# Kernel tuning notes

Hardware: AMD Instinct MI355X
Metric: run time of the kernel (lower is better)

## Reference

```python
import jax, jax.numpy as jnp
import numpy as np

NUM_HEADS = 8  # from init_kwargs


def setup_inputs() -> dict:
    key = jax.random.key(0)
    ks = jax.random.split(key, 8)
    B, N, Din, H, Dout, E = 4, 2048, 256, 512, 256, 65536
    s = 0.02
    return {
        "x": jax.random.normal(ks[0], (B, N, Din), jnp.float32),
        "edge_index": jax.random.randint(ks[1], (2, E), 0, N),
        "W_gcn": jax.random.normal(ks[2], (Din, H), jnp.float32) * s,
        "b_gcn": jnp.zeros((H,), jnp.float32),
        "in_proj_w": jax.random.normal(ks[3], (3 * H, H), jnp.float32) * s,
        "in_proj_b": jnp.zeros((3 * H,), jnp.float32),
        "out_proj_w": jax.random.normal(ks[4], (H, H), jnp.float32) * s,
        "out_proj_b": jnp.zeros((H,), jnp.float32),
        "fc_w": jax.random.normal(ks[5], (H, Dout), jnp.float32) * s,
        "fc_b": jnp.zeros((Dout,), jnp.float32),
    }


def _gcn(x, edge_index, W, b):
    # PyG GCNConv: add self-loops, symmetric normalization, gather-scatter aggregation.
    B, N, _ = x.shape
    loop = jnp.arange(N)
    src = jnp.concatenate([edge_index[0], loop])  # message source j
    dst = jnp.concatenate([edge_index[1], loop])  # aggregation target i
    deg = jnp.zeros((N,), x.dtype).at[dst].add(1.0)
    dinv = jnp.where(deg > 0, jax.lax.rsqrt(deg), 0.0)
    norm = dinv[src] * dinv[dst]                  # [Etot]
    xl = x @ W                                    # [B, N, H]
    msgs = xl[:, src, :] * norm[None, :, None]    # [B, Etot, H]
    out = jnp.zeros_like(xl).at[:, dst].add(msgs)  # scatter-add over edges
    return out + b


def _mha(x_nbh, wi, bi, wo, bo, nh):
    # torch MultiheadAttention, input [N(seq), B, H], self-attention.
    N, B, H = x_nbh.shape
    dh = H // nh
    qkv = x_nbh @ wi.T + bi                       # [N, B, 3H]
    q, k, v = jnp.split(qkv, 3, axis=-1)
    q = q.reshape(N, B, nh, dh) * (dh ** -0.5)
    k = k.reshape(N, B, nh, dh)
    v = v.reshape(N, B, nh, dh)
    scores = jnp.einsum("nbhd,mbhd->bhnm", q, k)  # [B, nh, N, N]
    attn = jax.nn.softmax(scores, axis=-1)
    o = jnp.einsum("bhnm,mbhd->nbhd", attn, v).reshape(N, B, H)
    return o @ wo.T + bo


def reference(x, edge_index, W_gcn, b_gcn, in_proj_w, in_proj_b,
              out_proj_w, out_proj_b, fc_w, fc_b):
    h = _gcn(x, edge_index, W_gcn, b_gcn)         # [B, N, H]
    h = jnp.transpose(h, (1, 0, 2))               # [N, B, H]
    h = _mha(h, in_proj_w, in_proj_b, out_proj_w, out_proj_b, NUM_HEADS)
    h = jnp.transpose(h, (1, 0, 2))               # [B, N, H]
    h = jax.nn.relu(h)
    return h @ fc_w + fc_b                        # [B, N, Dout]
```

## Files before the change

### kernel.cpp

```cpp
#include <hip/hip_runtime.h>
#include <hip/hip_bf16.h>


#define NN 2048
#define HH 512
#define NHEAD 8
#define DH 64

typedef _Float16 f16;
typedef __attribute__((ext_vector_type(2))) _Float16 f16x2;
typedef __attribute__((ext_vector_type(4))) _Float16 f16x4;
typedef __attribute__((ext_vector_type(8))) _Float16 f16x8;
typedef __attribute__((ext_vector_type(4))) float f32x4;

#define GLOAD_LDS16(g, l)                                              \
  __builtin_amdgcn_global_load_lds(                                    \
      (const __attribute__((address_space(1))) void*)(g),              \
      (__attribute__((address_space(3))) void*)(l), 16, 0, 0)


__global__ __launch_bounds__(256) void prep_cvt_kernel(const float* __restrict__ wi,
                                                       const float* __restrict__ wo,
                                                       f16* __restrict__ wi16,
                                                       f16* __restrict__ wo16,
                                                       float* __restrict__ deg,
                                                       int* __restrict__ cursor) {
  const int bid = blockIdx.x, t = threadIdx.x;
  if (bid < 768) {
    const int i = bid * 256 + t;
    const float4 v = ((const float4*)wi)[i];
    f16x4 o = { (f16)v.x, (f16)v.y, (f16)v.z, (f16)v.w };
    ((f16x4*)wi16)[i] = o;
  } else if (bid < 1024) {
    const int i = (bid - 768) * 256 + t;
    const float4 v = ((const float4*)wo)[i];
    f16x4 o = { (f16)v.x, (f16)v.y, (f16)v.z, (f16)v.w };
    ((f16x4*)wo16)[i] = o;
  } else {
    for (int i = t; i < NN; i += 256) { deg[i] = 1.0f; cursor[i] = 0; }
  }
}

__global__ __launch_bounds__(256) void prep_transpose_kernel(const float* __restrict__ wg,
                                                             const float* __restrict__ fcw,
                                                             f16* __restrict__ wg16t,
                                                             f16* __restrict__ fcw16t) {
  __shared__ float tbuf[32][33];
  const float* in;
  f16* outp;
  int R, C, bx, by;
  if (blockIdx.x < 128) { in = wg;  outp = wg16t;  R = 256; C = 512;
                          bx = blockIdx.x & 15; by = blockIdx.x >> 4; }
  else { int id = blockIdx.x - 128; in = fcw; outp = fcw16t; R = 512; C = 256;
         bx = id & 7; by = id >> 3; }
  const int c0 = bx * 32, r0 = by * 32;
  const int tx = threadIdx.x & 31, ty = threadIdx.x >> 5;
#pragma unroll
  for (int i = 0; i < 32; i += 8) tbuf[ty + i][tx] = in[(size_t)(r0 + ty + i) * C + c0 + tx];
  __syncthreads();
#pragma unroll
  for (int i = 0; i < 32; i += 8)
    outp[(size_t)(c0 + ty + i) * R + r0 + tx] = (f16)tbuf[tx][ty + i];
}


__global__ __launch_bounds__(256) void count_deg_kernel(const int* __restrict__ ei, int E,
                                                        float* __restrict__ deg) {
  int e = blockIdx.x * 256 + threadIdx.x;
  if (e < E) atomicAdd(&deg[ei[E + e]], 1.0f);
}

__global__ __launch_bounds__(1024) void build_rowptr_kernel(const float* __restrict__ deg,
                                                            float* __restrict__ dinv,
                                                            int* __restrict__ rowptr) {
  __shared__ int a[NN];
  __shared__ int bbuf[NN];
  const int t = threadIdx.x;
  for (int i = t; i < NN; i += 1024) {
    float dg = deg[i];
    a[i] = (int)dg - 1;
    dinv[i] = rsqrtf(dg);
  }
  __syncthreads();
  int* src = a;
  int* dst = bbuf;
  for (int off = 1; off < NN; off <<= 1) {
    for (int i = t; i < NN; i += 1024) {
      int v = src[i];
      if (i >= off) v += src[i - off];
      dst[i] = v;
    }
    __syncthreads();
    int* tmp = src; src = dst; dst = tmp;
  }
  for (int i = t; i < NN; i += 1024) rowptr[i + 1] = src[i];
  if (t == 0) rowptr[0] = 0;
}

__global__ __launch_bounds__(256) void fill_csr_kernel(const int* __restrict__ ei, int E,
                                                       const int* __restrict__ rowptr,
                                                       int* __restrict__ cursor,
                                                       int* __restrict__ csr_src) {
  int e = blockIdx.x * 256 + threadIdx.x;
  if (e < E) {
    int s = ei[e];
    int d = ei[E + e];
    int pos = atomicAdd(&cursor[d], 1);
    csr_src[rowptr[d] + pos] = s;
  }
}


template <int OUTMODE, bool BIAS, bool RELU, bool AF32, int MT = 128>
__global__ __launch_bounds__(256) void mfma_gemm_kernel(
    const void* __restrict__ Ap, const f16* __restrict__ Bt,
    const float* __restrict__ bias, void* __restrict__ Cout,
    int M, int N, int K,
    f16* __restrict__ q_out, f16* __restrict__ k_out, f16* __restrict__ v_out) {
  constexpr int MI = MT / 32;
  __shared__ f16 As[MT * 32];
  __shared__ f16 Bs[128 * 32];
  const int tid = threadIdx.x;
  const int wave = tid >> 6, lane = tid & 63;
  const int quad = lane >> 4, l16 = lane & 15;
  const int m0 = blockIdx.y * MT, n0 = blockIdx.x * 128;
  const int moff = (wave >> 1) * (MI * 16), noff = (wave & 1) * 64;

  f32x4 acc[MI][4];
#pragma unroll
  for (int i = 0; i < MI; ++i)
#pragma unroll
    for (int j = 0; j < 4; ++j) acc[i][j] = (f32x4){0.f, 0.f, 0.f, 0.f};

  const int rpw = MT / 4;
  const int srowA = rpw * wave + (lane >> 2);
  const int srowB = 32 * wave + (lane >> 2);
  const int kch = (lane & 3) * 8;
  const f16* Ag = (const f16*)Ap + (size_t)(m0 + srowA) * K + kch;
  const float* Ag32 = (const float*)Ap + (size_t)(m0 + srowA) * K + kch;
  const f16* Bg = Bt + (size_t)(n0 + srowB) * K + kch;
  f16* As_w = &As[(rpw * wave) * 32];
  f16* Bs_w = &Bs[(32 * wave) * 32];

  for (int k0 = 0; k0 < K; k0 += 32) {
    __syncthreads();
    if (AF32) {
#pragma unroll
      for (int t = 0; t < 2; ++t) {
        const float* g = Ag32 + k0 + (size_t)(16 * t) * K;
        const float4 u0 = *(const float4*)g;
        const float4 u1 = *(const float4*)(g + 4);
        f16x8 o = { (f16)u0.x, (f16)u0.y, (f16)u0.z, (f16)u0.w,
                    (f16)u1.x, (f16)u1.y, (f16)u1.z, (f16)u1.w };
        *(f16x8*)&As[(srowA + 16 * t) * 32 + kch] = o;
      }
    } else {
      GLOAD_LDS16(Ag + k0, As_w);
      if (MT == 128) GLOAD_LDS16(Ag + k0 + (size_t)16 * K, As_w + 16 * 32);
    }
    GLOAD_LDS16(Bg + k0, Bs_w);
    GLOAD_LDS16(Bg + k0 + (size_t)16 * K, Bs_w + 16 * 32);
    __syncthreads();
    f16x8 af[MI], bf[4];
#pragma unroll
    for (int m16 = 0; m16 < MI; ++m16)
      af[m16] = *(const f16x8*)&As[(moff + m16 * 16 + l16) * 32 + quad * 8];
#pragma unroll
    for (int n16 = 0; n16 < 4; ++n16)
      bf[n16] = *(const f16x8*)&Bs[(noff + n16 * 16 + l16) * 32 + quad * 8];
#pragma unroll
    for (int m16 = 0; m16 < MI; ++m16)
#pragma unroll
      for (int n16 = 0; n16 < 4; ++n16)
        acc[m16][n16] =
            __builtin_amdgcn_mfma_f32_16x16x32_f16(af[m16], bf[n16], acc[m16][n16], 0, 0, 0);
  }

  float bv[4];
#pragma unroll
  for (int n16 = 0; n16 < 4; ++n16)
    bv[n16] = BIAS ? bias[n0 + noff + n16 * 16 + l16] : 0.f;

  if (OUTMODE == 2) {
    const int hblk = (n0 >> 6) + (wave & 1);
    const int which = hblk >> 3, h = hblk & 7;
    f16* dst = (which == 0) ? q_out : (which == 1) ? k_out : v_out;
    const float scale = (which == 0) ? 0.125f : 1.0f;
#pragma unroll
    for (int m16 = 0; m16 < MI; ++m16) {
#pragma unroll
      for (int r = 0; r < 4; ++r) {
        const int m = m0 + moff + m16 * 16 + quad * 4 + r;
        const int b = m >> 11, ns = m & 2047;
        f16* row = dst + ((size_t)(b * 8 + h) * NN + ns) * DH;
#pragma unroll
        for (int n16 = 0; n16 < 4; ++n16) {
          const int d = n16 * 16 + l16;
          row[d] = (f16)((acc[m16][n16][r] + bv[n16]) * scale);
        }
      }
    }
  } else {
#pragma unroll
    for (int m16 = 0; m16 < MI; ++m16) {
#pragma unroll
      for (int r = 0; r < 4; ++r) {
        const size_t row = (size_t)(m0 + moff + m16 * 16 + quad * 4 + r) * N;
#pragma unroll
        for (int n16 = 0; n16 < 4; ++n16) {
          const int col = n0 + noff + n16 * 16 + l16;
          float v = acc[m16][n16][r] + bv[n16];
          if (RELU) v = fmaxf(v, 0.f);
          if (OUTMODE == 0) ((float*)Cout)[row + col] = v;
          else ((f16*)Cout)[row + col] = (f16)v;
        }
      }
    }
  }
}


__global__ __launch_bounds__(256) void gcn_aggregate_kernel(const f16* __restrict__ xl,
                                                            const float* __restrict__ dinv,
                                                            const int* __restrict__ rowptr,
                                                            const int* __restrict__ csr_src,
                                                            const float* __restrict__ b_gcn,
                                                            f16* __restrict__ out) {
  __shared__ int s_src[256];
  __shared__ float s_dv[256];
  const int i = blockIdx.x;
  const int tid = threadIdx.x;
  const float dv_i = dinv[i];
  const int f = tid * 2;
  float ax[4], ay[4];
#pragma unroll
  for (int b = 0; b < 4; ++b) {
    const f16x2 self = *(const f16x2*)&xl[((size_t)(b * NN) + i) * HH + f];
    ax[b] = (float)self.x * dv_i;
    ay[b] = (float)self.y * dv_i;
  }
  const int beg = rowptr[i], end = rowptr[i + 1];
  for (int c0 = beg; c0 < end; c0 += 256) {
    const int cnt = min(256, end - c0);
    __syncthreads();
    if (tid < cnt) {
      int s = csr_src[c0 + tid];
      s_src[tid] = s;
      s_dv[tid] = dinv[s];
    }
    __syncthreads();
    for (int t = 0; t < cnt; ++t) {
      const int row = s_src[t];
      const float w = s_dv[t];
#pragma unroll
      for (int b = 0; b < 4; ++b) {
        const f16x2 v = *(const f16x2*)&xl[((size_t)(b * NN) + row) * HH + f];
        ax[b] = fmaf((float)v.x, w, ax[b]);
        ay[b] = fmaf((float)v.y, w, ay[b]);
      }
    }
  }
  const float2 bg = *(const float2*)&b_gcn[f];
#pragma unroll
  for (int b = 0; b < 4; ++b) {
    f16x2 o = { (f16)(ax[b] * dv_i + bg.x), (f16)(ay[b] * dv_i + bg.y) };
    *(f16x2*)&out[((size_t)(b * NN) + i) * HH + f] = o;
  }
}


__global__ __launch_bounds__(256) void flash_attn_f16_kernel(const f16* __restrict__ Qb,
                                                             const f16* __restrict__ Kb,
                                                             const f16* __restrict__ Vb,
                                                             f16* __restrict__ out) {
  const int LDK = 72;
  const int LDV = 136;
  __shared__ f16 Ks[128 * LDK];
  __shared__ f16 Vt[64 * LDV];
  const int tid = threadIdx.x;
  const int wave = tid >> 6, lane = tid & 63;
  const int quad = lane >> 4, l16 = lane & 15;
  const int n0 = blockIdx.x * 128;
  const int bh = blockIdx.y;
  const int b = bh >> 3, h = bh & 7;
  const f16* kb = Kb + (size_t)bh * NN * DH;
  const f16* vb = Vb + (size_t)bh * NN * DH;

  f16x8 aq[2][2];
#pragma unroll
  for (int g = 0; g < 2; ++g) {
    const f16* qf = Qb + ((size_t)bh * NN + n0 + (wave + 4 * g) * 16 + l16) * DH + quad * 8;
    aq[g][0] = *(const f16x8*)qf;
    aq[g][1] = *(const f16x8*)(qf + 32);
  }

  float l_part[2] = {0.f, 0.f};
  f32x4 acc_o[2][4];
#pragma unroll
  for (int g = 0; g < 2; ++g)
#pragma unroll
    for (int n16 = 0; n16 < 4; ++n16) acc_o[g][n16] = (f32x4){0.f, 0.f, 0.f, 0.f};

  const int vdg = tid & 15, jbb = tid >> 4;

  for (int kt = 0; kt < NN / 128; ++kt) {
    const int k0 = kt * 128;
    __syncthreads();
#pragma unroll
    for (int i = 0; i < 4; ++i) {
      int idx = tid + 256 * i;
      int r = idx >> 3, koff = (idx & 7) * 8;
      *(f16x8*)&Ks[r * LDK + koff] = *(const f16x8*)(kb + (size_t)(k0 + r) * DH + koff);
    }
#pragma unroll
    for (int cc = 0; cc < 2; ++cc) {
      const int jb = jbb + 16 * cc;
      const int sb4 = (jb >> 3) * 32 + (jb & 3) * 8 + ((jb >> 2) & 1) * 4;
      f16x4 vv[4];
#pragma unroll
      for (int i = 0; i < 4; ++i)
        vv[i] = *(const f16x4*)(vb + (size_t)(k0 + jb * 4 + i) * DH + vdg * 4);
#pragma unroll
      for (int c = 0; c < 4; ++c) {
        f16x4 o = { vv[0][c], vv[1][c], vv[2][c], vv[3][c] };
        *(f16x4*)&Vt[(vdg * 4 + c) * LDV + sb4] = o;
      }
    }
    __syncthreads();
#pragma unroll
    for (int p = 0; p < 4; ++p) {
      f32x4 sA[2][2];
#pragma unroll
      for (int t = 0; t < 2; ++t) {
        const f16x8 ak0 = *(const f16x8*)&Ks[(p * 32 + t * 16 + l16) * LDK + quad * 8];
        const f16x8 ak1 = *(const f16x8*)&Ks[(p * 32 + t * 16 + l16) * LDK + quad * 8 + 32];
#pragma unroll
        for (int g = 0; g < 2; ++g) {
          f32x4 s = {0.f, 0.f, 0.f, 0.f};
          s = __builtin_amdgcn_mfma_f32_16x16x32_f16(ak0, aq[g][0], s, 0, 0, 0);
          s = __builtin_amdgcn_mfma_f32_16x16x32_f16(ak1, aq[g][1], s, 0, 0, 0);
          sA[g][t] = s;
        }
      }
      f16x8 bvv[4];
#pragma unroll
      for (int n16 = 0; n16 < 4; ++n16)
        bvv[n16] = *(const f16x8*)&Vt[(n16 * 16 + l16) * LDV + p * 32 + quad * 8];
#pragma unroll
      for (int g = 0; g < 2; ++g) {
        f16x8 ap;
        float sum = 0.f;
#pragma unroll
        for (int t = 0; t < 2; ++t)
#pragma unroll
          for (int r = 0; r < 4; ++r) {
            const float e = __expf(sA[g][t][r]);
            sum += e;
            ap[t * 4 + r] = (f16)e;
          }
        l_part[g] += sum;
#pragma unroll
        for (int n16 = 0; n16 < 4; ++n16)
          acc_o[g][n16] = __builtin_amdgcn_mfma_f32_16x16x32_f16(ap, bvv[n16], acc_o[g][n16], 0, 0, 0);
      }
    }
  }
#pragma unroll
  for (int g = 0; g < 2; ++g) {
    float lp = l_part[g];
    lp += __shfl_xor(lp, 16);
    lp += __shfl_xor(lp, 32);
    f16* obase = out + ((size_t)b * NN + n0 + (wave + 4 * g) * 16) * HH + h * DH;
#pragma unroll
    for (int r = 0; r < 4; ++r) {
      const float lr = __shfl(lp, (lane & 48) | (quad * 4 + r));
      const float inv = 1.0f / lr;
#pragma unroll
      for (int n16 = 0; n16 < 4; ++n16)
        obase[(size_t)(quad * 4 + r) * HH + n16 * 16 + l16] = (f16)(acc_o[g][n16][r] * inv);
    }
  }
}


extern "C" void kernel_launch(void* const* d_in, const int* in_sizes, int n_in,
                              void* d_out, int out_size, void* d_ws, size_t ws_size,
                              hipStream_t stream) {
  const float* x     = (const float*)d_in[0];
  const int*   ei    = (const int*)d_in[1];
  const float* W_gcn = (const float*)d_in[2];
  const float* b_gcn = (const float*)d_in[3];
  const float* wi    = (const float*)d_in[4];
  const float* bi    = (const float*)d_in[5];
  const float* wo    = (const float*)d_in[6];
  const float* bo    = (const float*)d_in[7];
  const float* fcw   = (const float*)d_in[8];
  const float* fcb   = (const float*)d_in[9];
  float* out = (float*)d_out;
  const int E = in_sizes[1] / 2;
  const int M = 4 * NN;

  char* wsb = (char*)d_ws;
  const size_t MB = 1u << 20;
  f16* xl16   = (f16*)(wsb + 4 * MB);
  f16* hb16   = (f16*)(wsb + 12 * MB);
  f16* Qb     = (f16*)(wsb + 20 * MB);
  f16* Kb     = (f16*)(wsb + 28 * MB);
  f16* Vb     = (f16*)(wsb + 36 * MB);
  f16* attn16 = (f16*)(wsb + 44 * MB);
  f16* proj16 = (f16*)(wsb + 52 * MB);
  f16* wi16   = (f16*)(wsb + 60 * MB);
  f16* wo16   = (f16*)(wsb + 62 * MB);
  f16* wg16t  = (f16*)(wsb + 63 * MB);
  f16* fcw16t = (f16*)(wsb + 64 * MB);
  float* deg  = (float*)(wsb + 65 * MB);
  float* dinv = deg + NN;
  int* rowptr = (int*)(dinv + NN);
  int* cursor = rowptr + 2080;
  int* csr    = cursor + NN;

  prep_cvt_kernel<<<1025, 256, 0, stream>>>(wi, wo, wi16, wo16, deg, cursor);
  prep_transpose_kernel<<<256, 256, 0, stream>>>(W_gcn, fcw, wg16t, fcw16t);

  count_deg_kernel<<<(E + 255) / 256, 256, 0, stream>>>(ei, E, deg);
  build_rowptr_kernel<<<1, 1024, 0, stream>>>(deg, dinv, rowptr);
  fill_csr_kernel<<<(E + 255) / 256, 256, 0, stream>>>(ei, E, rowptr, cursor, csr);

  mfma_gemm_kernel<1, false, false, true><<<dim3(4, 64), 256, 0, stream>>>(
      x, wg16t, nullptr, xl16, M, 512, 256, nullptr, nullptr, nullptr);
  gcn_aggregate_kernel<<<NN, 256, 0, stream>>>(xl16, dinv, rowptr, csr, b_gcn, hb16);
  mfma_gemm_kernel<2, true, false, false><<<dim3(12, 64), 256, 0, stream>>>(
      hb16, wi16, bi, nullptr, M, 1536, 512, Qb, Kb, Vb);
  flash_attn_f16_kernel<<<dim3(NN / 128, 32), 256, 0, stream>>>(Qb, Kb, Vb, attn16);
  mfma_gemm_kernel<1, true, true, false><<<dim3(4, 64), 256, 0, stream>>>(
      attn16, wo16, bo, proj16, M, 512, 512, nullptr, nullptr, nullptr);
  mfma_gemm_kernel<0, true, false, false, 64><<<dim3(2, 128), 256, 0, stream>>>(
      proj16, fcw16t, fcb, out, M, 256, 512, nullptr, nullptr, nullptr);
}
```

Measured before the change: 261.2 us.

## Restructure flash attention: 8 waves per block, register prefetch, exp2, XCD swizzle

Measured after the change: 258.0 us. About the same (-1.2%).

```diff
diff --git a/kernel.cpp b/kernel.cpp
--- a/kernel.cpp
+++ b/kernel.cpp
@@ -17,6 +17,23 @@
   __builtin_amdgcn_global_load_lds(                                    \
       (const __attribute__((address_space(1))) void*)(g),              \
       (__attribute__((address_space(3))) void*)(l), 16, 0, 0)
+
+__device__ __forceinline__ float fast_exp2(float x) {
+#if __has_builtin(__builtin_amdgcn_exp2f)
+  return __builtin_amdgcn_exp2f(x);
+#else
+  return exp2f(x);
+#endif
+}
+
+__device__ __forceinline__ f16x2 cvt_pk_f16(float a, float b) {
+#if __has_builtin(__builtin_amdgcn_cvt_pkrtz)
+  return __builtin_bit_cast(f16x2, __builtin_amdgcn_cvt_pkrtz(a, b));
+#else
+  f16x2 r = { (f16)a, (f16)b };
+  return r;
+#endif
+}
 
 
 __global__ __launch_bounds__(256) void prep_cvt_kernel(const float* __restrict__ wi,
@@ -185,7 +202,7 @@
     const int hblk = (n0 >> 6) + (wave & 1);
     const int which = hblk >> 3, h = hblk & 7;
     f16* dst = (which == 0) ? q_out : (which == 1) ? k_out : v_out;
-    const float scale = (which == 0) ? 0.125f : 1.0f;
+    const float scale = (which == 0) ? 0.125f * 1.44269504088896340736f : 1.0f;
 #pragma unroll
     for (int m16 = 0; m16 < MI; ++m16) {
 #pragma unroll
@@ -269,7 +286,7 @@
 }
 
 
-__global__ __launch_bounds__(256) void flash_attn_f16_kernel(const f16* __restrict__ Qb,
+__global__ __launch_bounds__(512) void flash_attn_f16_kernel(const f16* __restrict__ Qb,
                                                              const f16* __restrict__ Kb,
                                                              const f16* __restrict__ Vb,
                                                              f16* __restrict__ out) {
@@ -280,105 +297,102 @@
   const int tid = threadIdx.x;
   const int wave = tid >> 6, lane = tid & 63;
   const int quad = lane >> 4, l16 = lane & 15;
-  const int n0 = blockIdx.x * 128;
-  const int bh = blockIdx.y;
+  const int bid = blockIdx.x;
+  const int sw = (bid & 7) * 64 + (bid >> 3);
+  const int bh = sw >> 4;
+  const int n0 = (sw & 15) * 128;
   const int b = bh >> 3, h = bh & 7;
   const f16* kb = Kb + (size_t)bh * NN * DH;
   const f16* vb = Vb + (size_t)bh * NN * DH;
 
-  f16x8 aq[2][2];
-#pragma unroll
-  for (int g = 0; g < 2; ++g) {
-    const f16* qf = Qb + ((size_t)bh * NN + n0 + (wave + 4 * g) * 16 + l16) * DH + quad * 8;
-    aq[g][0] = *(const f16x8*)qf;
-    aq[g][1] = *(const f16x8*)(qf + 32);
-  }
-
-  float l_part[2] = {0.f, 0.f};
-  f32x4 acc_o[2][4];
-#pragma unroll
-  for (int g = 0; g < 2; ++g)
-#pragma unroll
-    for (int n16 = 0; n16 < 4; ++n16) acc_o[g][n16] = (f32x4){0.f, 0.f, 0.f, 0.f};
-
-  const int vdg = tid & 15, jbb = tid >> 4;
+  f16x8 aq0, aq1;
+  {
+    const f16* qf = Qb + ((size_t)bh * NN + n0 + wave * 16 + l16) * DH + quad * 8;
+    aq0 = *(const f16x8*)qf;
+    aq1 = *(const f16x8*)(qf + 32);
+  }
+
+  float l_part = 0.f;
+  f32x4 acc_o[4];
+#pragma unroll
+  for (int n16 = 0; n16 < 4; ++n16) acc_o[n16] = (f32x4){0.f, 0.f, 0.f, 0.f};
+
+  const int krow = tid >> 3, kcol = (tid & 7) * 8;
+  const int vdg = tid & 15, jb = tid >> 4;
+  const int sb4 = (jb >> 3) * 32 + (jb & 3) * 8 + ((jb >> 2) & 1) * 4;
+
+  f16x8 kreg0, kreg1;
+  f16x4 vreg[4];
+  {
+    kreg0 = *(const f16x8*)(kb + (size_t)krow * DH + kcol);
+    kreg1 = *(const f16x8*)(kb + (size_t)(64 + krow) * DH + kcol);
+#pragma unroll
+    for (int i = 0; i < 4; ++i)
+      vreg[i] = *(const f16x4*)(vb + (size_t)(jb * 4 + i) * DH + vdg * 4);
+  }
 
   for (int kt = 0; kt < NN / 128; ++kt) {
-    const int k0 = kt * 128;
-    __syncthreads();
-#pragma unroll
-    for (int i = 0; i < 4; ++i) {
-      int idx = tid + 256 * i;
-      int r = idx >> 3, koff = (idx & 7) * 8;
-      *(f16x8*)&Ks[r * LDK + koff] = *(const f16x8*)(kb + (size_t)(k0 + r) * DH + koff);
-    }
-#pragma unroll
-    for (int cc = 0; cc < 2; ++cc) {
-      const int jb = jbb + 16 * cc;
-      const int sb4 = (jb >> 3) * 32 + (jb & 3) * 8 + ((jb >> 2) & 1) * 4;
-      f16x4 vv[4];
+    __syncthreads();
+    *(f16x8*)&Ks[krow * LDK + kcol] = kreg0;
+    *(f16x8*)&Ks[(64 + krow) * LDK + kcol] = kreg1;
+#pragma unroll
+    for (int c = 0; c < 4; ++c) {
+      f16x4 o = { vreg[0][c], vreg[1][c], vreg[2][c], vreg[3][c] };
+      *(f16x4*)&Vt[(vdg * 4 + c) * LDV + sb4] = o;
+    }
+    if (kt + 1 < NN / 128) {
+      const int k0n = (kt + 1) * 128;
+      kreg0 = *(const f16x8*)(kb + (size_t)(k0n + krow) * DH + kcol);
+      kreg1 = *(const f16x8*)(kb + (size_t)(k0n + 64 + krow) * DH + kcol);
 #pragma unroll
       for (int i = 0; i < 4; ++i)
-        vv[i] = *(const f16x4*)(vb + (size_t)(k0 + jb * 4 + i) * DH + vdg * 4);
-#pragma unroll
-      for (int c = 0; c < 4; ++c) {
-        f16x4 o = { vv[0][c], vv[1][c], vv[2][c], vv[3][c] };
-        *(f16x4*)&Vt[(vdg * 4 + c) * LDV + sb4] = o;
-      }
+        vreg[i] = *(const f16x4*)(vb + (size_t)(k0n + jb * 4 + i) * DH + vdg * 4);
     }
     __syncthreads();
 #pragma unroll
     for (int p = 0; p < 4; ++p) {
-      f32x4 sA[2][2];
+      f32x4 sA[2];
 #pragma unroll
       for (int t = 0; t < 2; ++t) {
         const f16x8 ak0 = *(const f16x8*)&Ks[(p * 32 + t * 16 + l16) * LDK + quad * 8];
         const f16x8 ak1 = *(const f16x8*)&Ks[(p * 32 + t * 16 + l16) * LDK + quad * 8 + 32];
-#pragma unroll
-        for (int g = 0; g < 2; ++g) {
-          f32x4 s = {0.f, 0.f, 0.f, 0.f};
-          s = __builtin_amdgcn_mfma_f32_16x16x32_f16(ak0, aq[g][0], s, 0, 0, 0);
-          s = __builtin_amdgcn_mfma_f32_16x16x32_f16(ak1, aq[g][1], s, 0, 0, 0);
-          sA[g][t] = s;
-        }
+        f32x4 s = {0.f, 0.f, 0.f, 0.f};
+        s = __builtin_amdgcn_mfma_f32_16x16x32_f16(ak0, aq0, s, 0, 0, 0);
+        s = __builtin_amdgcn_mfma_f32_16x16x32_f16(ak1, aq1, s, 0, 0, 0);
+        sA[t] = s;
       }
       f16x8 bvv[4];
 #pragma unroll
       for (int n16 = 0; n16 < 4; ++n16)
         bvv[n16] = *(const f16x8*)&Vt[(n16 * 16 + l16) * LDV + p * 32 + quad * 8];
-#pragma unroll
-      for (int g = 0; g < 2; ++g) {
-        f16x8 ap;
-        float sum = 0.f;
-#pragma unroll
-        for (int t = 0; t < 2; ++t)
-#pragma unroll
-          for (int r = 0; r < 4; ++r) {
-            const float e = __expf(sA[g][t][r]);
-            sum += e;
-            ap[t * 4 + r] = (f16)e;
-          }
-        l_part[g] += sum;
-#pragma unroll
-        for (int n16 = 0; n16 < 4; ++n16)
-          acc_o[g][n16] = __builtin_amdgcn_mfma_f32_16x16x32_f16(ap, bvv[n16], acc_o[g][n16], 0, 0, 0);
-      }
-    }
-  }
-#pragma unroll
-  for (int g = 0; g < 2; ++g) {
-    float lp = l_part[g];
-    lp += __shfl_xor(lp, 16);
-    lp += __shfl_xor(lp, 32);
-    f16* obase = out + ((size_t)b * NN + n0 + (wave + 4 * g) * 16) * HH + h * DH;
-#pragma unroll
-    for (int r = 0; r < 4; ++r) {
-      const float lr = __shfl(lp, (lane & 48) | (quad * 4 + r));
-      const float inv = 1.0f / lr;
+      union { f16x8 v; f16x2 h[4]; } ap;
+      float sum = 0.f;
+#pragma unroll
+      for (int t = 0; t < 2; ++t)
+#pragma unroll
+        for (int rr = 0; rr < 2; ++rr) {
+          const float e0 = fast_exp2(sA[t][rr * 2]);
+          const float e1 = fast_exp2(sA[t][rr * 2 + 1]);
+          sum += e0 + e1;
+          ap.h[t * 2 + rr] = cvt_pk_f16(e0, e1);
+        }
+      l_part += sum;
 #pragma unroll
       for (int n16 = 0; n16 < 4; ++n16)
-        obase[(size_t)(quad * 4 + r) * HH + n16 * 16 + l16] = (f16)(acc_o[g][n16][r] * inv);
-    }
+        acc_o[n16] = __builtin_amdgcn_mfma_f32_16x16x32_f16(ap.v, bvv[n16], acc_o[n16], 0, 0, 0);
+    }
+  }
+  float lp = l_part;
+  lp += __shfl_xor(lp, 16);
+  lp += __shfl_xor(lp, 32);
+  f16* obase = out + ((size_t)b * NN + n0 + wave * 16) * HH + h * DH;
+#pragma unroll
+  for (int r = 0; r < 4; ++r) {
+    const float lr = __shfl(lp, (lane & 48) | (quad * 4 + r));
+    const float inv = 1.0f / lr;
+#pragma unroll
+    for (int n16 = 0; n16 < 4; ++n16)
+      obase[(size_t)(quad * 4 + r) * HH + n16 * 16 + l16] = (f16)(acc_o[n16][r] * inv);
   }
 }
 
@@ -431,7 +445,7 @@
   gcn_aggregate_kernel<<<NN, 256, 0, stream>>>(xl16, dinv, rowptr, csr, b_gcn, hb16);
   mfma_gemm_kernel<2, true, false, false><<<dim3(12, 64), 256, 0, stream>>>(
       hb16, wi16, bi, nullptr, M, 1536, 512, Qb, Kb, Vb);
-  flash_attn_f16_kernel<<<dim3(NN / 128, 32), 256, 0, stream>>>(Qb, Kb, Vb, attn16);
+  flash_attn_f16_kernel<<<512, 512, 0, stream>>>(Qb, Kb, Vb, attn16);
   mfma_gemm_kernel<1, true, true, false><<<dim3(4, 64), 256, 0, stream>>>(
       attn16, wo16, bo, proj16, M, 512, 512, nullptr, nullptr, nullptr);
   mfma_gemm_kernel<0, true, false, false, 64><<<dim3(2, 128), 256, 0, stream>>>(
```
